# Kernel tuning notes

Measured on AMD Instinct MI355X. Metric: run time of the kernel, lower is better.

The kernel has to match this reference:

```python
import jax, jax.numpy as jnp
import numpy as np

GRIDS = 7.0
L_COORD = 5.0
L_NOOBJ = 0.5


def setup_inputs() -> dict:
    key = jax.random.key(0)
    k1, k2 = jax.random.split(key)
    pred_tensor = jax.random.uniform(k1, (16384, 7, 7, 30), dtype=jnp.float32)
    target_tensor = jax.random.uniform(k2, (16384, 7, 7, 30), dtype=jnp.float32)
    return {"pred_tensor": pred_tensor, "target_tensor": target_tensor}


def _boxes(cx, cy, w, h, j, k):
    # cell-relative center -> absolute corner coords, as in the torch code:
    # x = (cx + j)/grids, y = (cy + k)/grids  (j indexes dim1, k indexes dim2)
    x = (cx + j) / GRIDS
    y = (cy + k) / GRIDS
    return x - w / 2, y - h / 2, x + w / 2, y + h / 2


def _iou(a, b):
    ix1 = jnp.maximum(a[0], b[0])
    iy1 = jnp.maximum(a[1], b[1])
    ix2 = jnp.minimum(a[2], b[2])
    iy2 = jnp.minimum(a[3], b[3])
    iw = jnp.maximum(ix2 - ix1, 0.0)
    ih = jnp.maximum(iy2 - iy1, 0.0)
    inter = iw * ih
    area_a = (a[2] - a[0]) * (a[3] - a[1])
    area_b = (b[2] - b[0]) * (b[3] - b[1])
    return jnp.where(inter > 0, inter / (area_a + area_b - inter), 0.0)


def _yolo_loss(p, t):
    B = p.shape[0]
    j = jnp.arange(7, dtype=p.dtype)[None, :, None]  # grid row index (dim 1)
    k = jnp.arange(7, dtype=p.dtype)[None, None, :]  # grid col index (dim 2)

    b1 = _boxes(p[..., 0], p[..., 1], p[..., 2], p[..., 3], j, k)
    b2 = _boxes(p[..., 5], p[..., 6], p[..., 7], p[..., 8], j, k)
    tb = _boxes(t[..., 0], t[..., 1], t[..., 2], t[..., 3], j, k)

    iou1 = _iou(b1, tb)  # [B,7,7]
    iou2 = _iou(b2, tb)

    obj = t[..., 4] > 0
    pick1 = iou1 >= iou2

    # coord + confidence loss if box1 is responsible
    coo1 = L_COORD * (
        jnp.sum((p[..., 0:2] - t[..., 0:2]) ** 2, axis=-1)
        + jnp.sum((jnp.sqrt(p[..., 2:4]) - jnp.sqrt(t[..., 2:4])) ** 2, axis=-1)
    ) + (p[..., 4] - iou1) ** 2
    non1 = L_NOOBJ * (p[..., 4] - iou2) ** 2

    # coord + confidence loss if box2 is responsible
    coo2 = L_COORD * (
        jnp.sum((p[..., 5:7] - t[..., 5:7]) ** 2, axis=-1)
        + jnp.sum((jnp.sqrt(p[..., 7:9]) - jnp.sqrt(t[..., 7:9])) ** 2, axis=-1)
    ) + (p[..., 9] - iou2) ** 2
    non2 = L_NOOBJ * (p[..., 9] - iou1) ** 2

    cls = jnp.sum((p[..., 10:] - t[..., 10:]) ** 2, axis=-1)
    noobj = L_NOOBJ * (p[..., 4] ** 2 + p[..., 9] ** 2)

    coo_loss = jnp.where(obj, jnp.where(pick1, coo1, coo2), 0.0)
    non_loss = jnp.where(obj, jnp.where(pick1, non1, non2), noobj)
    cls_loss = jnp.where(obj, cls, 0.0)

    total = jnp.sum(coo_loss + non_loss + cls_loss)
    return total / B


def reference(pred_tensor, target_tensor):
    return _yolo_loss(pred_tensor.astype(jnp.float32), target_tensor.astype(jnp.float32))
```

## Files before the change

kernel.cpp:

```cpp
#include <hip/hip_runtime.h>


#define NC 30
#define CPB 128
#define TILE_DW (CPB * NC)
#define CHUNKS 15

__device__ __forceinline__ float sq(float x) { return x * x; }

__device__ __forceinline__ void make_box(float cx, float cy, float w, float h,
                                         float jf, float kf, float b[4]) {
    float x = (cx + jf) * (1.0f / 7.0f);
    float y = (cy + kf) * (1.0f / 7.0f);
    b[0] = x - w * 0.5f;
    b[1] = y - h * 0.5f;
    b[2] = x + w * 0.5f;
    b[3] = y + h * 0.5f;
}

__device__ __forceinline__ float iou(const float a[4], const float b[4]) {
    float ix1 = fmaxf(a[0], b[0]);
    float iy1 = fmaxf(a[1], b[1]);
    float ix2 = fminf(a[2], b[2]);
    float iy2 = fminf(a[3], b[3]);
    float iw = fmaxf(ix2 - ix1, 0.0f);
    float ih = fmaxf(iy2 - iy1, 0.0f);
    float inter = iw * ih;
    float area_a = (a[2] - a[0]) * (a[3] - a[1]);
    float area_b = (b[2] - b[0]) * (b[3] - b[1]);
    return inter > 0.0f ? inter / (area_a + area_b - inter) : 0.0f;
}

__device__ __forceinline__ float cell_loss(const float* __restrict__ P,
                                           const float* __restrict__ T,
                                           float jf, float kf) {
    float b1[4], b2[4], tb[4];
    make_box(P[0], P[1], P[2], P[3], jf, kf, b1);
    make_box(P[5], P[6], P[7], P[8], jf, kf, b2);
    make_box(T[0], T[1], T[2], T[3], jf, kf, tb);

    float i1 = iou(b1, tb);
    float i2 = iou(b2, tb);

    bool obj = T[4] > 0.0f;
    bool pick1 = i1 >= i2;

    float cls = 0.0f;
#pragma unroll
    for (int e = 10; e < 30; ++e) {
        float d = P[e] - T[e];
        cls += d * d;
    }

    float coo1 = 5.0f * (sq(P[0] - T[0]) + sq(P[1] - T[1]) +
                         sq(sqrtf(P[2]) - sqrtf(T[2])) +
                         sq(sqrtf(P[3]) - sqrtf(T[3]))) +
                 sq(P[4] - i1);
    float non1 = 0.5f * sq(P[4] - i2);

    float coo2 = 5.0f * (sq(P[5] - T[5]) + sq(P[6] - T[6]) +
                         sq(sqrtf(P[7]) - sqrtf(T[7])) +
                         sq(sqrtf(P[8]) - sqrtf(T[8]))) +
                 sq(P[9] - i2);
    float non2 = 0.5f * sq(P[9] - i1);

    float noobj = 0.5f * (P[4] * P[4] + P[9] * P[9]);

    float resp = pick1 ? (coo1 + non1) : (coo2 + non2);
    return obj ? (resp + cls) : noobj;
}

template <bool USE_WS>
__global__ __launch_bounds__(CPB) void yolo_partial_kernel(
    const float* __restrict__ pred, const float* __restrict__ targ,
    float* __restrict__ dst, int ncells, float scale) {
    __shared__ float sp[TILE_DW];
    __shared__ float st[TILE_DW];

    int t = threadIdx.x;
    int wave = t >> 6;
    int lane = t & 63;
    int base = blockIdx.x * CPB;
    int cell = base + t;

    bool full_tile = (base + CPB) <= ncells;

    float loss = 0.0f;

    if (full_tile) {
        const float* pbase = pred + (size_t)base * NC;
        const float* tbase = targ + (size_t)base * NC;

        for (int c = wave; c < CHUNKS; c += 2) {
            __builtin_amdgcn_global_load_lds(
                (const __attribute__((address_space(1))) unsigned int*)(pbase + c * 256 + lane * 4),
                (__attribute__((address_space(3))) unsigned int*)(sp + c * 256),
                16, 0, 0);
            __builtin_amdgcn_global_load_lds(
                (const __attribute__((address_space(1))) unsigned int*)(tbase + c * 256 + lane * 4),
                (__attribute__((address_space(3))) unsigned int*)(st + c * 256),
                16, 0, 0);
        }
        __syncthreads();

        int jc = (cell / 7) % 7;
        int kc = cell % 7;
        loss = cell_loss(sp + t * NC, st + t * NC, (float)jc, (float)kc);
    } else if (cell < ncells) {
        float P[NC], T[NC];
        const float* pp = pred + (size_t)cell * NC;
        const float* tt = targ + (size_t)cell * NC;
#pragma unroll
        for (int e = 0; e < NC; ++e) {
            P[e] = pp[e];
            T[e] = tt[e];
        }
        int jc = (cell / 7) % 7;
        int kc = cell % 7;
        loss = cell_loss(P, T, (float)jc, (float)kc);
    }

#pragma unroll
    for (int off = 32; off > 0; off >>= 1) loss += __shfl_down(loss, off);

    __shared__ float wsum[CPB / 64];
    if (lane == 0) wsum[wave] = loss;
    __syncthreads();

    if (t == 0) {
        float s = 0.0f;
#pragma unroll
        for (int w = 0; w < CPB / 64; ++w) s += wsum[w];
        if (USE_WS) {
            dst[blockIdx.x] = s * scale;
        } else {
            atomicAdd(dst, s * scale);
        }
    }
}

__global__ __launch_bounds__(1024) void reduce_kernel(
    const float* __restrict__ ws, float* __restrict__ out, int n) {
    float s = 0.0f;
    for (int i = threadIdx.x; i < n; i += 1024) s += ws[i];
#pragma unroll
    for (int off = 32; off > 0; off >>= 1) s += __shfl_down(s, off);

    __shared__ float acc[16];
    int wave = threadIdx.x >> 6;
    int lane = threadIdx.x & 63;
    if (lane == 0) acc[wave] = s;
    __syncthreads();

    if (threadIdx.x == 0) {
        float tot = 0.0f;
#pragma unroll
        for (int w = 0; w < 16; ++w) tot += acc[w];
        out[0] = tot;
    }
}

extern "C" void kernel_launch(void* const* d_in, const int* in_sizes, int n_in,
                              void* d_out, int out_size, void* d_ws, size_t ws_size,
                              hipStream_t stream) {
    const float* pred = (const float*)d_in[0];
    const float* targ = (const float*)d_in[1];
    float* out = (float*)d_out;

    int ncells = in_sizes[0] / NC;
    int batch = ncells / 49;
    float inv_b = 1.0f / (float)batch;

    int grid = (ncells + CPB - 1) / CPB;

    if (ws_size >= (size_t)grid * sizeof(float)) {
        float* ws = (float*)d_ws;
        yolo_partial_kernel<true><<<grid, CPB, 0, stream>>>(pred, targ, ws,
                                                            ncells, inv_b);
        reduce_kernel<<<1, 1024, 0, stream>>>(ws, out, grid);
    } else {
        hipMemsetAsync(out, 0, sizeof(float), stream);
        yolo_partial_kernel<false><<<grid, CPB, 0, stream>>>(pred, targ, out,
                                                             ncells, inv_b);
    }
}
```

Measured before the change: 36.19 us.

## Use persistent single-wave blocks with double-buffered LDS tile prefetch

```diff
diff --git a/kernel.cpp b/kernel.cpp
--- a/kernel.cpp
+++ b/kernel.cpp
@@ -2,11 +2,36 @@
 
 
 #define NC 30
-#define CPB 128
-#define TILE_DW (CPB * NC)
-#define CHUNKS 15
+#define TPW 64
+#define TILE_DW (TPW * NC)
+#define MAXGRID 1280
 
 __device__ __forceinline__ float sq(float x) { return x * x; }
+
+__device__ __forceinline__ void g16(const float* g, float* l) {
+    __builtin_amdgcn_global_load_lds(
+        (const __attribute__((address_space(1))) unsigned int*)g,
+        (__attribute__((address_space(3))) unsigned int*)l, 16, 0, 0);
+}
+__device__ __forceinline__ void g4(const float* g, float* l) {
+    __builtin_amdgcn_global_load_lds(
+        (const __attribute__((address_space(1))) unsigned int*)g,
+        (__attribute__((address_space(3))) unsigned int*)l, 4, 0, 0);
+}
+
+__device__ __forceinline__ void stage_tile(const float* pb, const float* tb,
+                                           float* sp, float* st, int lane) {
+#pragma unroll
+    for (int c = 0; c < 7; ++c) {
+        g16(pb + c * 256 + lane * 4, sp + c * 256);
+        g16(tb + c * 256 + lane * 4, st + c * 256);
+    }
+#pragma unroll
+    for (int p = 0; p < 2; ++p) {
+        g4(pb + 1792 + p * 64 + lane, sp + 1792 + p * 64);
+        g4(tb + 1792 + p * 64 + lane, st + 1792 + p * 64);
+    }
+}
 
 __device__ __forceinline__ void make_box(float cx, float cy, float w, float h,
                                          float jf, float kf, float b[4]) {
@@ -70,73 +95,65 @@
     return obj ? (resp + cls) : noobj;
 }
 
-template <bool USE_WS>
-__global__ __launch_bounds__(CPB) void yolo_partial_kernel(
+__global__ __launch_bounds__(64) void yolo_partial_kernel(
     const float* __restrict__ pred, const float* __restrict__ targ,
-    float* __restrict__ dst, int ncells, float scale) {
-    __shared__ float sp[TILE_DW];
-    __shared__ float st[TILE_DW];
-
-    int t = threadIdx.x;
-    int wave = t >> 6;
-    int lane = t & 63;
-    int base = blockIdx.x * CPB;
-    int cell = base + t;
-
-    bool full_tile = (base + CPB) <= ncells;
-
-    float loss = 0.0f;
-
-    if (full_tile) {
-        const float* pbase = pred + (size_t)base * NC;
-        const float* tbase = targ + (size_t)base * NC;
-
-        for (int c = wave; c < CHUNKS; c += 2) {
-            __builtin_amdgcn_global_load_lds(
-                (const __attribute__((address_space(1))) unsigned int*)(pbase + c * 256 + lane * 4),
-                (__attribute__((address_space(3))) unsigned int*)(sp + c * 256),
-                16, 0, 0);
-            __builtin_amdgcn_global_load_lds(
-                (const __attribute__((address_space(1))) unsigned int*)(tbase + c * 256 + lane * 4),
-                (__attribute__((address_space(3))) unsigned int*)(st + c * 256),
-                16, 0, 0);
+    float* __restrict__ ws, int ncells, float scale) {
+    __shared__ float sp[2][TILE_DW];
+    __shared__ float st[2][TILE_DW];
+
+    int lane = threadIdx.x;
+    int bid = blockIdx.x;
+    int nb = gridDim.x;
+    int ntiles = ncells / TPW;
+
+    float acc = 0.0f;
+    int cur = 0;
+
+    if (bid < ntiles)
+        stage_tile(pred + (size_t)bid * TILE_DW, targ + (size_t)bid * TILE_DW,
+                   sp[0], st[0], lane);
+
+    for (int t = bid; t < ntiles; t += nb) {
+        int tn = t + nb;
+        if (tn < ntiles) {
+            stage_tile(pred + (size_t)tn * TILE_DW,
+                       targ + (size_t)tn * TILE_DW, sp[cur ^ 1], st[cur ^ 1],
+                       lane);
+            asm volatile("s_waitcnt vmcnt(18)" ::: "memory");
+        } else {
+            asm volatile("s_waitcnt vmcnt(0)" ::: "memory");
         }
-        __syncthreads();
-
-        int jc = (cell / 7) % 7;
-        int kc = cell % 7;
-        loss = cell_loss(sp + t * NC, st + t * NC, (float)jc, (float)kc);
-    } else if (cell < ncells) {
+        __builtin_amdgcn_sched_barrier(0);
+
+        const float* P = sp[cur] + lane * NC;
+        const float* T = st[cur] + lane * NC;
+        int cell = t * TPW + lane;
+        int q7 = cell / 7;
+        int kc = cell - q7 * 7;
+        int jc = q7 % 7;
+        acc += cell_loss(P, T, (float)jc, (float)kc);
+        __builtin_amdgcn_sched_barrier(0);
+        cur ^= 1;
+    }
+
+    int rem = ncells - ntiles * TPW;
+    if (rem > 0 && bid == 0 && lane < rem) {
         float P[NC], T[NC];
-        const float* pp = pred + (size_t)cell * NC;
-        const float* tt = targ + (size_t)cell * NC;
+        const float* pp = pred + (size_t)(ntiles * TPW + lane) * NC;
+        const float* tt = targ + (size_t)(ntiles * TPW + lane) * NC;
 #pragma unroll
         for (int e = 0; e < NC; ++e) {
             P[e] = pp[e];
             T[e] = tt[e];
         }
-        int jc = (cell / 7) % 7;
-        int kc = cell % 7;
-        loss = cell_loss(P, T, (float)jc, (float)kc);
-    }
-
-#pragma unroll
-    for (int off = 32; off > 0; off >>= 1) loss += __shfl_down(loss, off);
-
-    __shared__ float wsum[CPB / 64];
-    if (lane == 0) wsum[wave] = loss;
-    __syncthreads();
-
-    if (t == 0) {
-        float s = 0.0f;
-#pragma unroll
-        for (int w = 0; w < CPB / 64; ++w) s += wsum[w];
-        if (USE_WS) {
-            dst[blockIdx.x] = s * scale;
-        } else {
-            atomicAdd(dst, s * scale);
-        }
-    }
+        int cell = ntiles * TPW + lane;
+        int q7 = cell / 7;
+        acc += cell_loss(P, T, (float)(q7 % 7), (float)(cell - q7 * 7));
+    }
+
+#pragma unroll
+    for (int off = 32; off > 0; off >>= 1) acc += __shfl_down(acc, off);
+    if (lane == 0) ws[bid] = acc * scale;
 }
 
 __global__ __launch_bounds__(1024) void reduce_kernel(
@@ -171,16 +188,15 @@
     int batch = ncells / 49;
     float inv_b = 1.0f / (float)batch;
 
-    int grid = (ncells + CPB - 1) / CPB;
-
-    if (ws_size >= (size_t)grid * sizeof(float)) {
-        float* ws = (float*)d_ws;
-        yolo_partial_kernel<true><<<grid, CPB, 0, stream>>>(pred, targ, ws,
-                                                            ncells, inv_b);
-        reduce_kernel<<<1, 1024, 0, stream>>>(ws, out, grid);
-    } else {
-        hipMemsetAsync(out, 0, sizeof(float), stream);
-        yolo_partial_kernel<false><<<grid, CPB, 0, stream>>>(pred, targ, out,
-                                                             ncells, inv_b);
-    }
-}
+    int ntiles = ncells / TPW;
+    int nb = ntiles < MAXGRID ? (ntiles > 0 ? ntiles : 1) : MAXGRID;
+    size_t need = (size_t)nb * sizeof(float);
+    if (ws_size < need) {
+        int cap = (int)(ws_size / sizeof(float));
+        nb = cap > 0 ? cap : 1;
+    }
+
+    float* ws = (float*)d_ws;
+    yolo_partial_kernel<<<nb, TPW, 0, stream>>>(pred, targ, ws, ncells, inv_b);
+    reduce_kernel<<<1, 1024, 0, stream>>>(ws, out, nb);
+}
```

After: 36.50 us. Within noise of the previous version (+0.9%).

## Replace LDS staging with direct coord loads and coalesced masked class-loss pass

Applied to the files above, without the earlier changes.

```diff
diff --git a/kernel.cpp b/kernel.cpp
--- a/kernel.cpp
+++ b/kernel.cpp
@@ -2,9 +2,11 @@
 
 
 #define NC 30
-#define CPB 128
+#define CPB 256
 #define TILE_DW (CPB * NC)
-#define CHUNKS 15
+
+typedef float f4 __attribute__((ext_vector_type(4), aligned(4)));
+typedef float f2 __attribute__((ext_vector_type(2), aligned(8)));
 
 __device__ __forceinline__ float sq(float x) { return x * x; }
 
@@ -31,9 +33,8 @@
     return inter > 0.0f ? inter / (area_a + area_b - inter) : 0.0f;
 }
 
-__device__ __forceinline__ float cell_loss(const float* __restrict__ P,
-                                           const float* __restrict__ T,
-                                           float jf, float kf) {
+__device__ __forceinline__ float coord_loss(const float P[10], const float T[10],
+                                            float jf, float kf, bool* objp) {
     float b1[4], b2[4], tb[4];
     make_box(P[0], P[1], P[2], P[3], jf, kf, b1);
     make_box(P[5], P[6], P[7], P[8], jf, kf, b2);
@@ -44,13 +45,7 @@
 
     bool obj = T[4] > 0.0f;
     bool pick1 = i1 >= i2;
-
-    float cls = 0.0f;
-#pragma unroll
-    for (int e = 10; e < 30; ++e) {
-        float d = P[e] - T[e];
-        cls += d * d;
-    }
+    *objp = obj;
 
     float coo1 = 5.0f * (sq(P[0] - T[0]) + sq(P[1] - T[1]) +
                          sq(sqrtf(P[2]) - sqrtf(T[2])) +
@@ -67,70 +62,114 @@
     float noobj = 0.5f * (P[4] * P[4] + P[9] * P[9]);
 
     float resp = pick1 ? (coo1 + non1) : (coo2 + non2);
-    return obj ? (resp + cls) : noobj;
+    return obj ? resp : noobj;
+}
+
+__device__ __forceinline__ void load10(const float* row, float P[10]) {
+    f2 a = *reinterpret_cast<const f2*>(row + 0);
+    f2 b = *reinterpret_cast<const f2*>(row + 2);
+    f2 c = *reinterpret_cast<const f2*>(row + 4);
+    f2 d = *reinterpret_cast<const f2*>(row + 6);
+    f2 e = *reinterpret_cast<const f2*>(row + 8);
+    P[0] = a.x; P[1] = a.y; P[2] = b.x; P[3] = b.y; P[4] = c.x;
+    P[5] = c.y; P[6] = d.x; P[7] = d.y; P[8] = e.x; P[9] = e.y;
 }
 
 template <bool USE_WS>
-__global__ __launch_bounds__(CPB) void yolo_partial_kernel(
+__global__ __launch_bounds__(CPB, 6) void yolo_partial_kernel(
     const float* __restrict__ pred, const float* __restrict__ targ,
     float* __restrict__ dst, int ncells, float scale) {
-    __shared__ float sp[TILE_DW];
-    __shared__ float st[TILE_DW];
+    __shared__ float maskv[CPB];
+    __shared__ float wsum[CPB / 64];
 
     int t = threadIdx.x;
+    int base = blockIdx.x * CPB;
+    int cell = base + t;
+    bool full_tile = (base + CPB) <= ncells;
+
+    float acc = 0.0f;
+
+    if (full_tile) {
+        {
+            float P[10], T[10];
+            load10(pred + (size_t)cell * NC, P);
+            load10(targ + (size_t)cell * NC, T);
+            int q7 = cell / 7;
+            int kc = cell - q7 * 7;
+            int jc = q7 % 7;
+            bool obj;
+            acc = coord_loss(P, T, (float)jc, (float)kc, &obj);
+            maskv[t] = obj ? 1.0f : 0.0f;
+        }
+        __syncthreads();
+
+        const float* pb = pred + (size_t)base * NC;
+        const float* tb = targ + (size_t)base * NC;
+
+#pragma unroll
+        for (int i = 0; i < 7; ++i) {
+            int idx = i * 1024 + 4 * t;
+            f4 p = *reinterpret_cast<const f4*>(pb + idx);
+            f4 q = *reinterpret_cast<const f4*>(tb + idx);
+            int c0 = idx / 30;
+            int ch = idx - 30 * c0;
+#pragma unroll
+            for (int e = 0; e < 4; ++e) {
+                int che = ch + e;
+                int over = che >= 30;
+                int ce = c0 + over;
+                che -= 30 * over;
+                float w = (che >= 10) ? maskv[ce] : 0.0f;
+                float d = p[e] - q[e];
+                acc += w * d * d;
+            }
+        }
+        {
+            int idx = 7168 + 2 * t;
+            f2 p = *reinterpret_cast<const f2*>(pb + idx);
+            f2 q = *reinterpret_cast<const f2*>(tb + idx);
+            int c0 = idx / 30;
+            int ch = idx - 30 * c0;
+#pragma unroll
+            for (int e = 0; e < 2; ++e) {
+                int che = ch + e;
+                int over = che >= 30;
+                int ce = c0 + over;
+                che -= 30 * over;
+                float w = (che >= 10) ? maskv[ce] : 0.0f;
+                float d = p[e] - q[e];
+                acc += w * d * d;
+            }
+        }
+    } else if (cell < ncells) {
+        float P[10], T[10];
+        load10(pred + (size_t)cell * NC, P);
+        load10(targ + (size_t)cell * NC, T);
+        int q7 = cell / 7;
+        bool obj;
+        acc = coord_loss(P, T, (float)(q7 % 7), (float)(cell - q7 * 7), &obj);
+        if (obj) {
+            const float* pp = pred + (size_t)cell * NC;
+            const float* tt = targ + (size_t)cell * NC;
+            float cls = 0.0f;
+#pragma unroll
+            for (int e = 10; e < 30; ++e) {
+                float d = pp[e] - tt[e];
+                cls += d * d;
+            }
+            acc += cls;
+        }
+    }
+
+#pragma unroll
+    for (int off = 32; off > 0; off >>= 1) acc += __shfl_down(acc, off);
     int wave = t >> 6;
     int lane = t & 63;
-    int base = blockIdx.x * CPB;
-    int cell = base + t;
-
-    bool full_tile = (base + CPB) <= ncells;
-
-    float loss = 0.0f;
-
-    if (full_tile) {
-        const float* pbase = pred + (size_t)base * NC;
-        const float* tbase = targ + (size_t)base * NC;
-
-        for (int c = wave; c < CHUNKS; c += 2) {
-            __builtin_amdgcn_global_load_lds(
-                (const __attribute__((address_space(1))) unsigned int*)(pbase + c * 256 + lane * 4),
-                (__attribute__((address_space(3))) unsigned int*)(sp + c * 256),
-                16, 0, 0);
-            __builtin_amdgcn_global_load_lds(
-                (const __attribute__((address_space(1))) unsigned int*)(tbase + c * 256 + lane * 4),
-                (__attribute__((address_space(3))) unsigned int*)(st + c * 256),
-                16, 0, 0);
-        }
-        __syncthreads();
-
-        int jc = (cell / 7) % 7;
-        int kc = cell % 7;
-        loss = cell_loss(sp + t * NC, st + t * NC, (float)jc, (float)kc);
-    } else if (cell < ncells) {
-        float P[NC], T[NC];
-        const float* pp = pred + (size_t)cell * NC;
-        const float* tt = targ + (size_t)cell * NC;
-#pragma unroll
-        for (int e = 0; e < NC; ++e) {
-            P[e] = pp[e];
-            T[e] = tt[e];
-        }
-        int jc = (cell / 7) % 7;
-        int kc = cell % 7;
-        loss = cell_loss(P, T, (float)jc, (float)kc);
-    }
-
-#pragma unroll
-    for (int off = 32; off > 0; off >>= 1) loss += __shfl_down(loss, off);
-
-    __shared__ float wsum[CPB / 64];
-    if (lane == 0) wsum[wave] = loss;
+    if (lane == 0) wsum[wave] = acc;
     __syncthreads();
 
     if (t == 0) {
-        float s = 0.0f;
-#pragma unroll
-        for (int w = 0; w < CPB / 64; ++w) s += wsum[w];
+        float s = wsum[0] + wsum[1] + wsum[2] + wsum[3];
         if (USE_WS) {
             dst[blockIdx.x] = s * scale;
         } else {
```

Result: slower. 79.51 us (+119.7%).

## Split each cell across 8 lanes with vector loads and grid-stride loop

Applied to the files above, without the earlier changes.

```diff
diff --git a/kernel.cpp b/kernel.cpp
--- a/kernel.cpp
+++ b/kernel.cpp
@@ -2,9 +2,8 @@
 
 
 #define NC 30
-#define CPB 128
-#define TILE_DW (CPB * NC)
-#define CHUNKS 15
+
+typedef float f4 __attribute__((ext_vector_type(4), aligned(4)));
 
 __device__ __forceinline__ float sq(float x) { return x * x; }
 
@@ -31,106 +30,121 @@
     return inter > 0.0f ? inter / (area_a + area_b - inter) : 0.0f;
 }
 
-__device__ __forceinline__ float cell_loss(const float* __restrict__ P,
-                                           const float* __restrict__ T,
-                                           float jf, float kf) {
-    float b1[4], b2[4], tb[4];
-    make_box(P[0], P[1], P[2], P[3], jf, kf, b1);
-    make_box(P[5], P[6], P[7], P[8], jf, kf, b2);
-    make_box(T[0], T[1], T[2], T[3], jf, kf, tb);
-
-    float i1 = iou(b1, tb);
-    float i2 = iou(b2, tb);
-
-    bool obj = T[4] > 0.0f;
-    bool pick1 = i1 >= i2;
-
-    float cls = 0.0f;
-#pragma unroll
-    for (int e = 10; e < 30; ++e) {
-        float d = P[e] - T[e];
-        cls += d * d;
-    }
-
-    float coo1 = 5.0f * (sq(P[0] - T[0]) + sq(P[1] - T[1]) +
-                         sq(sqrtf(P[2]) - sqrtf(T[2])) +
-                         sq(sqrtf(P[3]) - sqrtf(T[3]))) +
-                 sq(P[4] - i1);
-    float non1 = 0.5f * sq(P[4] - i2);
-
-    float coo2 = 5.0f * (sq(P[5] - T[5]) + sq(P[6] - T[6]) +
-                         sq(sqrtf(P[7]) - sqrtf(T[7])) +
-                         sq(sqrtf(P[8]) - sqrtf(T[8]))) +
-                 sq(P[9] - i2);
-    float non2 = 0.5f * sq(P[9] - i1);
-
-    float noobj = 0.5f * (P[4] * P[4] + P[9] * P[9]);
-
-    float resp = pick1 ? (coo1 + non1) : (coo2 + non2);
-    return obj ? (resp + cls) : noobj;
-}
-
 template <bool USE_WS>
-__global__ __launch_bounds__(CPB) void yolo_partial_kernel(
+__global__ __launch_bounds__(256) void yolo_partial_kernel(
     const float* __restrict__ pred, const float* __restrict__ targ,
     float* __restrict__ dst, int ncells, float scale) {
-    __shared__ float sp[TILE_DW];
-    __shared__ float st[TILE_DW];
-
     int t = threadIdx.x;
+    int j = t & 7;
+    int gbase = t & ~7;
+    int nchunks = (ncells + 31) / 32;
+    int total_dw = ncells * NC;
+
+    float acc = 0.0f;
+
+    for (int chunk = blockIdx.x; chunk < nchunks; chunk += gridDim.x) {
+        int cell = chunk * 32 + (t >> 3);
+        bool cell_ok = cell < ncells;
+
+        int dwbase = cell * NC + 4 * j;
+        int ldbase = dwbase;
+        int shift = 0;
+        if (cell_ok && dwbase + 4 > total_dw) {
+            ldbase = total_dw - 4;
+            shift = dwbase - ldbase;
+        }
+
+        f4 Pv = {0.f, 0.f, 0.f, 0.f}, Tv = {0.f, 0.f, 0.f, 0.f};
+        if (cell_ok) {
+            Pv = *reinterpret_cast<const f4*>(pred + ldbase);
+            Tv = *reinterpret_cast<const f4*>(targ + ldbase);
+        }
+        if (shift) {
+            f4 p2 = Pv, t2 = Tv;
+#pragma unroll
+            for (int e = 0; e < 4; ++e) {
+                int src = e + shift;
+                p2[e] = (src < 4) ? Pv[src] : 0.f;
+                t2[e] = (src < 4) ? Tv[src] : 0.f;
+            }
+            Pv = p2;
+            Tv = t2;
+        }
+
+        float t4 = __shfl(Tv[0], gbase + 1, 64);
+        float objw = t4 > 0.0f ? 1.0f : 0.0f;
+
+        float cls = 0.0f;
+#pragma unroll
+        for (int e = 0; e < 4; ++e) {
+            int ch = 4 * j + e;
+            float d = Pv[e] - Tv[e];
+            cls += (ch >= 10 && ch < 30) ? d * d : 0.0f;
+        }
+        acc += objw * cls;
+
+        float s1p[4], s2p[4], s1t[4], s2t[4];
+#pragma unroll
+        for (int e = 0; e < 4; ++e) {
+            s1p[e] = __shfl(Pv[e], gbase + 1, 64);
+            s2p[e] = __shfl(Pv[e], gbase + 2, 64);
+            s1t[e] = __shfl(Tv[e], gbase + 1, 64);
+            s2t[e] = __shfl(Tv[e], gbase + 2, 64);
+        }
+
+        if (j == 0 && cell_ok) {
+            float P0 = Pv[0], P1 = Pv[1], P2 = Pv[2], P3 = Pv[3];
+            float P4 = s1p[0], P5 = s1p[1], P6 = s1p[2], P7 = s1p[3];
+            float P8 = s2p[0], P9 = s2p[1];
+            float T0 = Tv[0], T1 = Tv[1], T2 = Tv[2], T3 = Tv[3];
+            float T4 = s1t[0], T5 = s1t[1], T6 = s1t[2], T7 = s1t[3];
+            float T8 = s2t[0];
+
+            int q7 = cell / 7;
+            float kf = (float)(cell - q7 * 7);
+            float jf = (float)(q7 % 7);
+
+            float b1[4], b2[4], tb[4];
+            make_box(P0, P1, P2, P3, jf, kf, b1);
+            make_box(P5, P6, P7, P8, jf, kf, b2);
+            make_box(T0, T1, T2, T3, jf, kf, tb);
+
+            float i1 = iou(b1, tb);
+            float i2 = iou(b2, tb);
+
+            bool obj = T4 > 0.0f;
+            bool pick1 = i1 >= i2;
+
+            float coo1 = 5.0f * (sq(P0 - T0) + sq(P1 - T1) +
+                                 sq(sqrtf(P2) - sqrtf(T2)) +
+                                 sq(sqrtf(P3) - sqrtf(T3))) +
+                         sq(P4 - i1);
+            float non1 = 0.5f * sq(P4 - i2);
+
+            float coo2 = 5.0f * (sq(P5 - T5) + sq(P6 - T6) +
+                                 sq(sqrtf(P7) - sqrtf(T7)) +
+                                 sq(sqrtf(P8) - sqrtf(T8))) +
+                         sq(P9 - i2);
+            float non2 = 0.5f * sq(P9 - i1);
+
+            float noobj = 0.5f * (P4 * P4 + P9 * P9);
+
+            float resp = pick1 ? (coo1 + non1) : (coo2 + non2);
+            acc += obj ? resp : noobj;
+        }
+    }
+
+#pragma unroll
+    for (int off = 32; off > 0; off >>= 1) acc += __shfl_down(acc, off);
+
+    __shared__ float wsum[4];
     int wave = t >> 6;
     int lane = t & 63;
-    int base = blockIdx.x * CPB;
-    int cell = base + t;
-
-    bool full_tile = (base + CPB) <= ncells;
-
-    float loss = 0.0f;
-
-    if (full_tile) {
-        const float* pbase = pred + (size_t)base * NC;
-        const float* tbase = targ + (size_t)base * NC;
-
-        for (int c = wave; c < CHUNKS; c += 2) {
-            __builtin_amdgcn_global_load_lds(
-                (const __attribute__((address_space(1))) unsigned int*)(pbase + c * 256 + lane * 4),
-                (__attribute__((address_space(3))) unsigned int*)(sp + c * 256),
-                16, 0, 0);
-            __builtin_amdgcn_global_load_lds(
-                (const __attribute__((address_space(1))) unsigned int*)(tbase + c * 256 + lane * 4),
-                (__attribute__((address_space(3))) unsigned int*)(st + c * 256),
-                16, 0, 0);
-        }
-        __syncthreads();
-
-        int jc = (cell / 7) % 7;
-        int kc = cell % 7;
-        loss = cell_loss(sp + t * NC, st + t * NC, (float)jc, (float)kc);
-    } else if (cell < ncells) {
-        float P[NC], T[NC];
-        const float* pp = pred + (size_t)cell * NC;
-        const float* tt = targ + (size_t)cell * NC;
-#pragma unroll
-        for (int e = 0; e < NC; ++e) {
-            P[e] = pp[e];
-            T[e] = tt[e];
-        }
-        int jc = (cell / 7) % 7;
-        int kc = cell % 7;
-        loss = cell_loss(P, T, (float)jc, (float)kc);
-    }
-
-#pragma unroll
-    for (int off = 32; off > 0; off >>= 1) loss += __shfl_down(loss, off);
-
-    __shared__ float wsum[CPB / 64];
-    if (lane == 0) wsum[wave] = loss;
+    if (lane == 0) wsum[wave] = acc;
     __syncthreads();
 
     if (t == 0) {
-        float s = 0.0f;
-#pragma unroll
-        for (int w = 0; w < CPB / 64; ++w) s += wsum[w];
+        float s = wsum[0] + wsum[1] + wsum[2] + wsum[3];
         if (USE_WS) {
             dst[blockIdx.x] = s * scale;
         } else {
@@ -171,16 +185,17 @@
     int batch = ncells / 49;
     float inv_b = 1.0f / (float)batch;
 
-    int grid = (ncells + CPB - 1) / CPB;
+    int nchunks = (ncells + 31) / 32;
+    int grid = nchunks < 2048 ? nchunks : 2048;
 
     if (ws_size >= (size_t)grid * sizeof(float)) {
         float* ws = (float*)d_ws;
-        yolo_partial_kernel<true><<<grid, CPB, 0, stream>>>(pred, targ, ws,
+        yolo_partial_kernel<true><<<grid, 256, 0, stream>>>(pred, targ, ws,
                                                             ncells, inv_b);
         reduce_kernel<<<1, 1024, 0, stream>>>(ws, out, grid);
     } else {
         hipMemsetAsync(out, 0, sizeof(float), stream);
-        yolo_partial_kernel<false><<<grid, CPB, 0, stream>>>(pred, targ, out,
+        yolo_partial_kernel<false><<<grid, 256, 0, stream>>>(pred, targ, out,
                                                              ncells, inv_b);
     }
 }
```

New measurement: 54.17 us. 1.5x slower.
